# Performance work log

Measured on AMD Instinct MI355X. Metric: run time of the kernel, lower is better.

The kernel has to match this reference:

```python
import jax, jax.numpy as jnp
import numpy as np

ORDER = 256
THETA = 23.0
HIDDEN = 512
INPUT_DIM = 256
BATCH = 8192
TIMESTEPS = 23
LEAKY_SLOPE = 0.2  # tf.nn.leaky_relu default alpha


def _expm_np(M):
    # scaling-and-squaring + Taylor series, float64 numpy (replaces scipy expm)
    n = M.shape[0]
    nrm = np.linalg.norm(M, 1)
    s = max(0, int(np.ceil(np.log2(max(nrm, 1e-30)))) + 1)
    Ms = M / (2.0 ** s)
    E = np.eye(n)
    term = np.eye(n)
    for k in range(1, 30):
        term = term @ Ms / k
        E = E + term
    for _ in range(s):
        E = E @ E
    return E


def get_state_space_matrices(order, theta):
    Q = np.arange(order, dtype=np.float64)
    R = (2 * Q + 1)[:, None] / theta
    j, i = np.meshgrid(Q, Q)
    A = np.where(i < j, -1, (-1.0) ** (i - j + 1)) * R
    B = (-1.0) ** Q[:, None] * R
    # zero-order-hold discretization with dt=1: expm of augmented matrix
    aug = np.zeros((order + 1, order + 1))
    aug[:order, :order] = A
    aug[:order, order:] = B
    M = _expm_np(aug)
    return M[:order, :order], M[:order, order:]


def setup_inputs() -> dict:
    key = jax.random.key(0)
    ks = jax.random.split(key, 5)
    A_np, B_np = get_state_space_matrices(ORDER, THETA)

    def glorot(k, shape):
        lim = np.sqrt(6.0 / (shape[0] + shape[1]))
        return jax.random.uniform(k, shape, jnp.float32, -lim, lim)

    return {
        "inputs": jax.random.normal(ks[0], (BATCH, TIMESTEPS, INPUT_DIM), jnp.float32),
        "A": jnp.asarray(A_np, jnp.float32),          # [order, order]
        "B": jnp.asarray(B_np, jnp.float32),          # [order, 1]
        "W_h": glorot(ks[1], (HIDDEN, HIDDEN)),
        "W_m": glorot(ks[2], (HIDDEN, ORDER)),
        "W_x": glorot(ks[3], (INPUT_DIM, HIDDEN)),
        "e_x": glorot(ks[4], (INPUT_DIM, 1)),
    }


def reference(inputs, A, B, W_h, W_m, W_x, e_x):
    batch = inputs.shape[0]
    Bv = B[:, 0]  # [order]

    def step(carry, x_t):  # x_t: [batch, input_dim]
        h, m = carry  # h: [batch, hidden], m: [batch, order]
        u = x_t @ e_x  # [batch, 1]
        m_new = m @ A.T + u * Bv[None, :]          # [batch, order]
        pre = x_t @ W_x + h @ W_h.T + m_new @ W_m.T  # [batch, hidden]
        h_new = jnp.where(pre >= 0, pre, LEAKY_SLOPE * pre)
        return (h_new, m_new), h_new

    h0 = jnp.zeros((batch, W_h.shape[0]), inputs.dtype)
    m0 = jnp.zeros((batch, A.shape[0]), inputs.dtype)
    xs = jnp.transpose(inputs, (1, 0, 2))  # [T, batch, input_dim]
    _, hs = jax.lax.scan(step, (h0, m0), xs)
    return jnp.transpose(hs, (1, 0, 2))  # [batch, T, hidden]
```

## Files before the change

### kernel.cpp

```cpp
#include <hip/hip_runtime.h>

#define T_STEPS 23
#define ORD 256
#define HID 512
#define IN_DIM 256
#define NBATCH 8192
#define SLOPE 0.2f
#define LDH (T_STEPS * HID)
#define ROWS 32

__device__ __forceinline__ float lrelu(float x) { return x >= 0.f ? x : SLOPE * x; }

__device__ __forceinline__ ushort f2bf(float x) {
    unsigned u = __float_as_uint(x);
    u += 0x7fffu + ((u >> 16) & 1u);
    return (ushort)(u >> 16);
}
__device__ __forceinline__ float bf2f(ushort h) { return __uint_as_float((unsigned)h << 16); }

typedef __attribute__((ext_vector_type(8))) short bf16x8;
typedef __attribute__((ext_vector_type(4))) float f32x4;

__device__ __forceinline__ f32x4 nt_load4(const float* p) {
    return __builtin_nontemporal_load((const f32x4*)p);
}
__device__ __forceinline__ void nt_store4(float* p, f32x4 v) {
    __builtin_nontemporal_store(v, (f32x4*)p);
}

__global__ void vchain_kernel(const float* __restrict__ A,
                              const float* __restrict__ Bv,
                              float* __restrict__ V) {
    __shared__ float v[ORD];
    int i = threadIdx.x;
    v[i] = Bv[i];
    __syncthreads();
    for (int k = 0; k < T_STEPS; ++k) {
        V[k * ORD + i] = v[i];
        float a = 0.f;
        const float4* ar = (const float4*)(A + i * ORD);
        const float4* vr = (const float4*)v;
        #pragma unroll 8
        for (int t = 0; t < ORD / 4; ++t) {
            float4 a4 = ar[t];
            float4 v4 = vr[t];
            a += a4.x * v4.x + a4.y * v4.y + a4.z * v4.z + a4.w * v4.w;
        }
        __syncthreads();
        v[i] = a;
        __syncthreads();
    }
}

__global__ void wtab_kernel(const float* __restrict__ Wm,
                            const float* __restrict__ V,
                            float* __restrict__ wtab) {
    __shared__ float vs[ORD];
    int k = blockIdx.x;
    int j = blockIdx.y * 64 + threadIdx.x;
    ((float4*)vs)[threadIdx.x] = ((const float4*)(V + k * ORD))[threadIdx.x];
    __syncthreads();
    float a = 0.f;
    const float4* wr = (const float4*)(Wm + j * ORD);
    const float4* vr = (const float4*)vs;
    #pragma unroll 8
    for (int i = 0; i < ORD / 4; ++i) {
        float4 w4 = wr[i];
        float4 v4 = vr[i];
        a += w4.x * v4.x + w4.y * v4.y + w4.z * v4.z + w4.w * v4.w;
    }
    wtab[k * HID + j] = a;
}

__global__ void u_kernel(const float* __restrict__ X,
                         const float* __restrict__ ex,
                         float* __restrict__ u) {
    int row = blockIdx.x * 4 + (threadIdx.x >> 6);
    int lane = threadIdx.x & 63;
    const float4* xp = (const float4*)(X + (size_t)row * IN_DIM);
    const float4* ep = (const float4*)ex;
    float4 x4 = xp[lane];
    float4 e4 = ep[lane];
    float acc = x4.x * e4.x + x4.y * e4.y + x4.z * e4.z + x4.w * e4.w;
    #pragma unroll
    for (int off = 32; off; off >>= 1) acc += __shfl_down(acc, off);
    if (lane == 0) u[row] = acc;
}

__global__ __launch_bounds__(256) void gemm_xwx(const float* __restrict__ X,
                                                const float* __restrict__ Wx,
                                                float* __restrict__ out) {
    __shared__ float As[16][68];
    __shared__ float Bs[16][68];
    int tid = threadIdx.x;
    int row0 = blockIdx.x * 64;
    int col0 = blockIdx.y * 64;
    int tx = tid & 15, ty = tid >> 4;
    int am = tid >> 2, ak4 = tid & 3;
    float acc[4][4] = {};
    for (int k0 = 0; k0 < 256; k0 += 16) {
        float4 av = *(const float4*)(X + (size_t)(row0 + am) * IN_DIM + k0 + ak4 * 4);
        float4 bv = *(const float4*)(Wx + (size_t)(k0 + ty) * HID + col0 + tx * 4);
        __syncthreads();
        As[ak4 * 4 + 0][am] = av.x;
        As[ak4 * 4 + 1][am] = av.y;
        As[ak4 * 4 + 2][am] = av.z;
        As[ak4 * 4 + 3][am] = av.w;
        *(float4*)&Bs[ty][tx * 4] = bv;
        __syncthreads();
        #pragma unroll
        for (int kk = 0; kk < 16; ++kk) {
            float4 a4 = *(const float4*)&As[kk][ty * 4];
            float4 b4 = *(const float4*)&Bs[kk][tx * 4];
            float a[4] = {a4.x, a4.y, a4.z, a4.w};
            float b[4] = {b4.x, b4.y, b4.z, b4.w};
            #pragma unroll
            for (int i = 0; i < 4; ++i)
                #pragma unroll
                for (int j = 0; j < 4; ++j)
                    acc[i][j] += a[i] * b[j];
        }
    }
    #pragma unroll
    for (int i = 0; i < 4; ++i) {
        float4 v = make_float4(acc[i][0], acc[i][1], acc[i][2], acc[i][3]);
        *(float4*)(out + (size_t)(row0 + ty * 4 + i) * HID + col0 + tx * 4) = v;
    }
}

__global__ __launch_bounds__(512) void memconv_kernel(const float* __restrict__ u,
                                                      const float* __restrict__ wtab,
                                                      float* __restrict__ out) {
    int b = blockIdx.x, j = threadIdx.x;
    __shared__ float us[T_STEPS];
    if (j < T_STEPS) us[j] = u[b * T_STEPS + j];
    float w[T_STEPS];
    #pragma unroll
    for (int k = 0; k < T_STEPS; ++k) w[k] = wtab[k * HID + j];
    __syncthreads();
    float* ob = out + (size_t)b * LDH + j;
    #pragma unroll
    for (int t = 0; t < T_STEPS; ++t) {
        float acc = 0.f;
        #pragma unroll
        for (int s = 0; s <= t; ++s) acc += us[s] * w[t - s];
        ob[t * HID] += acc;
    }
}

__global__ void whpack_kernel(const float* __restrict__ Wh,
                              ushort* __restrict__ whi,
                              ushort* __restrict__ wlo) {
    int f = blockIdx.x;
    int s = blockIdx.y;
    int l = threadIdx.x;
    int n = f * 16 + (l & 15);
    int k0 = s * 32 + 4 * (l >> 4);
    float4 a = *(const float4*)(Wh + (size_t)n * HID + k0);
    float4 b = *(const float4*)(Wh + (size_t)n * HID + k0 + 16);
    float v[8] = {a.x, a.y, a.z, a.w, b.x, b.y, b.z, b.w};
    unsigned hp[4], lp[4];
    #pragma unroll
    for (int e2 = 0; e2 < 4; ++e2) {
        ushort h0 = f2bf(v[2 * e2]),     h1 = f2bf(v[2 * e2 + 1]);
        ushort l0 = f2bf(v[2 * e2]     - bf2f(h0));
        ushort l1 = f2bf(v[2 * e2 + 1] - bf2f(h1));
        hp[e2] = (unsigned)h0 | ((unsigned)h1 << 16);
        lp[e2] = (unsigned)l0 | ((unsigned)l1 << 16);
    }
    size_t off = ((size_t)(f * 16 + s) * 64 + l) * 8;
    *(uint4*)(whi + off) = make_uint4(hp[0], hp[1], hp[2], hp[3]);
    *(uint4*)(wlo + off) = make_uint4(lp[0], lp[1], lp[2], lp[3]);
}


__device__ __forceinline__ bf16x8 ld_frag(const ushort* base, int o1, int o2) {
    ushort4 p = *(const ushort4*)(base + o1);
    ushort4 q = *(const ushort4*)(base + o2);
    bf16x8 r;
    r[0] = (short)p.x; r[1] = (short)p.y; r[2] = (short)p.z; r[3] = (short)p.w;
    r[4] = (short)q.x; r[5] = (short)q.y; r[6] = (short)q.z; r[7] = (short)q.w;
    return r;
}

__device__ __forceinline__ void store_hilo(ushort* hhi, ushort* hlo, int off, f32x4 v) {
    ushort h0 = f2bf(v[0]), h1 = f2bf(v[1]), h2 = f2bf(v[2]), h3 = f2bf(v[3]);
    *(ushort4*)(hhi + off) = make_ushort4(h0, h1, h2, h3);
    ushort l0 = f2bf(v[0] - bf2f(h0));
    ushort l1 = f2bf(v[1] - bf2f(h1));
    ushort l2 = f2bf(v[2] - bf2f(h2));
    ushort l3 = f2bf(v[3] - bf2f(h3));
    *(ushort4*)(hlo + off) = make_ushort4(l0, l1, l2, l3);
}

__global__ __launch_bounds__(1024) void rec_fused(const ushort* __restrict__ whi,
                                                  const ushort* __restrict__ wlo,
                                                  float* __restrict__ out) {
    __shared__ ushort hbuf[2][2][ROWS * 512];
    const int tid = threadIdx.x;
    const int w  = tid >> 6;
    const int l  = tid & 63;
    const int lm = l & 15;
    const int g  = l >> 4;
    const int row0 = blockIdx.x * ROWS;
    const int xsw = lm << 2;

    float* obase[2];
    obase[0] = out + (size_t)(row0 + lm) * LDH + w * 32 + 4 * g;
    obase[1] = out + (size_t)(row0 + 16 + lm) * LDH + w * 32 + 4 * g;

    #pragma unroll
    for (int bi = 0; bi < 2; ++bi) {
        #pragma unroll
        for (int jf = 0; jf < 2; ++jf) {
            f32x4 vv = nt_load4(obase[bi] + jf * 16);
            vv[0] = lrelu(vv[0]); vv[1] = lrelu(vv[1]);
            vv[2] = lrelu(vv[2]); vv[3] = lrelu(vv[3]);
            nt_store4(obase[bi] + jf * 16, vv);
            int m  = bi * 16 + lm;
            int nb = w * 32 + jf * 16 + 4 * g;
            store_hilo(&hbuf[0][0][0], &hbuf[0][1][0], m * 512 + (nb ^ xsw), vv);
        }
    }

    const ushort* wh_l = whi + (size_t)w * 16384 + (size_t)l * 8;
    const ushort* wl_l = wlo + (size_t)w * 16384 + (size_t)l * 8;

    int buf = 0;
    #pragma unroll 1
    for (int t = 1; t < T_STEPS; ++t) {
        f32x4 pregs[2][2];
        #pragma unroll
        for (int jf = 0; jf < 2; ++jf)
            #pragma unroll
            for (int bi = 0; bi < 2; ++bi)
                pregs[jf][bi] = nt_load4(obase[bi] + t * HID + jf * 16);

        __syncthreads();

        const ushort* hh = &hbuf[buf][0][0];
        const ushort* hl = &hbuf[buf][1][0];
        f32x4 acc[2][2] = {};

        #pragma unroll
        for (int s = 0; s < 16; ++s) {
            bf16x8 ah[2], al[2], bh[2], bl[2];
            #pragma unroll
            for (int jf = 0; jf < 2; ++jf) {
                ah[jf] = *(const bf16x8*)(wh_l + jf * 8192 + s * 512);
                al[jf] = *(const bf16x8*)(wl_l + jf * 8192 + s * 512);
            }
            #pragma unroll
            for (int bi = 0; bi < 2; ++bi) {
                int m  = bi * 16 + lm;
                int o1 = m * 512 + ((s * 32 + 4 * g)      ^ xsw);
                int o2 = m * 512 + ((s * 32 + 16 + 4 * g) ^ xsw);
                bh[bi] = ld_frag(hh, o1, o2);
                bl[bi] = ld_frag(hl, o1, o2);
            }
            #pragma unroll
            for (int jf = 0; jf < 2; ++jf)
                #pragma unroll
                for (int bi = 0; bi < 2; ++bi) {
                    acc[jf][bi] = __builtin_amdgcn_mfma_f32_16x16x32_bf16(ah[jf], bh[bi], acc[jf][bi], 0, 0, 0);
                    acc[jf][bi] = __builtin_amdgcn_mfma_f32_16x16x32_bf16(ah[jf], bl[bi], acc[jf][bi], 0, 0, 0);
                    acc[jf][bi] = __builtin_amdgcn_mfma_f32_16x16x32_bf16(al[jf], bh[bi], acc[jf][bi], 0, 0, 0);
                }
        }

        buf ^= 1;
        #pragma unroll
        for (int jf = 0; jf < 2; ++jf)
            #pragma unroll
            for (int bi = 0; bi < 2; ++bi) {
                f32x4 r;
                r[0] = lrelu(acc[jf][bi][0] + pregs[jf][bi][0]);
                r[1] = lrelu(acc[jf][bi][1] + pregs[jf][bi][1]);
                r[2] = lrelu(acc[jf][bi][2] + pregs[jf][bi][2]);
                r[3] = lrelu(acc[jf][bi][3] + pregs[jf][bi][3]);
                nt_store4(obase[bi] + t * HID + jf * 16, r);
                int m  = bi * 16 + lm;
                int nb = w * 32 + jf * 16 + 4 * g;
                store_hilo(&hbuf[buf][0][0], &hbuf[buf][1][0], m * 512 + (nb ^ xsw), r);
            }
    }
}

extern "C" void kernel_launch(void* const* d_in, const int* in_sizes, int n_in,
                              void* d_out, int out_size, void* d_ws, size_t ws_size,
                              hipStream_t stream) {
    const float* X  = (const float*)d_in[0];
    const float* A  = (const float*)d_in[1];
    const float* Bv = (const float*)d_in[2];
    const float* Wh = (const float*)d_in[3];
    const float* Wm = (const float*)d_in[4];
    const float* Wx = (const float*)d_in[5];
    const float* ex = (const float*)d_in[6];
    float* out = (float*)d_out;

    float* u    = (float*)d_ws;
    float* V    = u + NBATCH * T_STEPS;
    float* wtab = V + T_STEPS * ORD;
    ushort* whp_hi = (ushort*)(wtab + T_STEPS * HID);
    ushort* whp_lo = whp_hi + HID * HID;

    const int nrows = NBATCH * T_STEPS;

    vchain_kernel<<<1, 256, 0, stream>>>(A, Bv, V);
    wtab_kernel<<<dim3(T_STEPS, HID / 64), 64, 0, stream>>>(Wm, V, wtab);
    whpack_kernel<<<dim3(HID / 16, HID / 32), 64, 0, stream>>>(Wh, whp_hi, whp_lo);

    u_kernel<<<nrows / 4, 256, 0, stream>>>(X, ex, u);

    gemm_xwx<<<dim3(nrows / 64, HID / 64), 256, 0, stream>>>(X, Wx, out);

    memconv_kernel<<<NBATCH, HID, 0, stream>>>(u, wtab, out);

    rec_fused<<<NBATCH / ROWS, 1024, 0, stream>>>(whp_hi, whp_lo, out);
}
```

Before: 2.591 ms.

## Replace FP32 input GEMM and memory convolution with fused split-bf16 MFMA kernel

Replaces the scalar FP32 X@W_x GEMM and the separate memory-convolution kernel with one MFMA kernel. It packs W_x and the convolution table into hi/lo bf16 fragments and expresses the causal convolution over u as an extra K=32 MFMA slice per row tile. This removes the read-modify-write pass over the output and moves the dominant GEMM onto matrix cores using a three-product hi/lo split to keep near-FP32 accuracy. The recurrent kernel also changes to 512 threads with wider per-wave column tiles and register double-buffering of W_h fragments, which raises register pressure.

```diff
diff --git a/kernel.cpp b/kernel.cpp
--- a/kernel.cpp
+++ b/kernel.cpp
@@ -8,6 +8,7 @@
 #define SLOPE 0.2f
 #define LDH (T_STEPS * HID)
 #define ROWS 32
+#define PRB 64
 
 __device__ __forceinline__ float lrelu(float x) { return x >= 0.f ? x : SLOPE * x; }
 
@@ -21,9 +22,30 @@
 typedef __attribute__((ext_vector_type(8))) short bf16x8;
 typedef __attribute__((ext_vector_type(4))) float f32x4;
 
-__device__ __forceinline__ f32x4 nt_load4(const float* p) {
-    return __builtin_nontemporal_load((const f32x4*)p);
-}
+
+__device__ __forceinline__ bf16x8 ld_frag(const ushort* base, int o1, int o2) {
+    ushort4 p = *(const ushort4*)(base + o1);
+    ushort4 q = *(const ushort4*)(base + o2);
+    bf16x8 r;
+    r[0] = (short)p.x; r[1] = (short)p.y; r[2] = (short)p.z; r[3] = (short)p.w;
+    r[4] = (short)q.x; r[5] = (short)q.y; r[6] = (short)q.z; r[7] = (short)q.w;
+    return r;
+}
+
+__device__ __forceinline__ void store_hilo(ushort* hhi, ushort* hlo, int off, f32x4 v) {
+    ushort h0 = f2bf(v[0]), h1 = f2bf(v[1]), h2 = f2bf(v[2]), h3 = f2bf(v[3]);
+    *(ushort4*)(hhi + off) = make_ushort4(h0, h1, h2, h3);
+    ushort l0 = f2bf(v[0] - bf2f(h0));
+    ushort l1 = f2bf(v[1] - bf2f(h1));
+    ushort l2 = f2bf(v[2] - bf2f(h2));
+    ushort l3 = f2bf(v[3] - bf2f(h3));
+    *(ushort4*)(hlo + off) = make_ushort4(l0, l1, l2, l3);
+}
+
+__device__ __forceinline__ void split_hilo(float x, ushort& hi, ushort& lo) {
+    hi = f2bf(x); lo = f2bf(x - bf2f(hi));
+}
+
 __device__ __forceinline__ void nt_store4(float* p, f32x4 v) {
     __builtin_nontemporal_store(v, (f32x4*)p);
 }
@@ -87,73 +109,10 @@
     if (lane == 0) u[row] = acc;
 }
 
-__global__ __launch_bounds__(256) void gemm_xwx(const float* __restrict__ X,
-                                                const float* __restrict__ Wx,
-                                                float* __restrict__ out) {
-    __shared__ float As[16][68];
-    __shared__ float Bs[16][68];
-    int tid = threadIdx.x;
-    int row0 = blockIdx.x * 64;
-    int col0 = blockIdx.y * 64;
-    int tx = tid & 15, ty = tid >> 4;
-    int am = tid >> 2, ak4 = tid & 3;
-    float acc[4][4] = {};
-    for (int k0 = 0; k0 < 256; k0 += 16) {
-        float4 av = *(const float4*)(X + (size_t)(row0 + am) * IN_DIM + k0 + ak4 * 4);
-        float4 bv = *(const float4*)(Wx + (size_t)(k0 + ty) * HID + col0 + tx * 4);
-        __syncthreads();
-        As[ak4 * 4 + 0][am] = av.x;
-        As[ak4 * 4 + 1][am] = av.y;
-        As[ak4 * 4 + 2][am] = av.z;
-        As[ak4 * 4 + 3][am] = av.w;
-        *(float4*)&Bs[ty][tx * 4] = bv;
-        __syncthreads();
-        #pragma unroll
-        for (int kk = 0; kk < 16; ++kk) {
-            float4 a4 = *(const float4*)&As[kk][ty * 4];
-            float4 b4 = *(const float4*)&Bs[kk][tx * 4];
-            float a[4] = {a4.x, a4.y, a4.z, a4.w};
-            float b[4] = {b4.x, b4.y, b4.z, b4.w};
-            #pragma unroll
-            for (int i = 0; i < 4; ++i)
-                #pragma unroll
-                for (int j = 0; j < 4; ++j)
-                    acc[i][j] += a[i] * b[j];
-        }
-    }
-    #pragma unroll
-    for (int i = 0; i < 4; ++i) {
-        float4 v = make_float4(acc[i][0], acc[i][1], acc[i][2], acc[i][3]);
-        *(float4*)(out + (size_t)(row0 + ty * 4 + i) * HID + col0 + tx * 4) = v;
-    }
-}
-
-__global__ __launch_bounds__(512) void memconv_kernel(const float* __restrict__ u,
-                                                      const float* __restrict__ wtab,
-                                                      float* __restrict__ out) {
-    int b = blockIdx.x, j = threadIdx.x;
-    __shared__ float us[T_STEPS];
-    if (j < T_STEPS) us[j] = u[b * T_STEPS + j];
-    float w[T_STEPS];
-    #pragma unroll
-    for (int k = 0; k < T_STEPS; ++k) w[k] = wtab[k * HID + j];
-    __syncthreads();
-    float* ob = out + (size_t)b * LDH + j;
-    #pragma unroll
-    for (int t = 0; t < T_STEPS; ++t) {
-        float acc = 0.f;
-        #pragma unroll
-        for (int s = 0; s <= t; ++s) acc += us[s] * w[t - s];
-        ob[t * HID] += acc;
-    }
-}
-
 __global__ void whpack_kernel(const float* __restrict__ Wh,
                               ushort* __restrict__ whi,
                               ushort* __restrict__ wlo) {
-    int f = blockIdx.x;
-    int s = blockIdx.y;
-    int l = threadIdx.x;
+    int f = blockIdx.x, s = blockIdx.y, l = threadIdx.x;
     int n = f * 16 + (l & 15);
     int k0 = s * 32 + 4 * (l >> 4);
     float4 a = *(const float4*)(Wh + (size_t)n * HID + k0);
@@ -162,9 +121,9 @@
     unsigned hp[4], lp[4];
     #pragma unroll
     for (int e2 = 0; e2 < 4; ++e2) {
-        ushort h0 = f2bf(v[2 * e2]),     h1 = f2bf(v[2 * e2 + 1]);
-        ushort l0 = f2bf(v[2 * e2]     - bf2f(h0));
-        ushort l1 = f2bf(v[2 * e2 + 1] - bf2f(h1));
+        ushort h0, l0, h1, l1;
+        split_hilo(v[2 * e2], h0, l0);
+        split_hilo(v[2 * e2 + 1], h1, l1);
         hp[e2] = (unsigned)h0 | ((unsigned)h1 << 16);
         lp[e2] = (unsigned)l0 | ((unsigned)l1 << 16);
     }
@@ -173,104 +132,229 @@
     *(uint4*)(wlo + off) = make_uint4(lp[0], lp[1], lp[2], lp[3]);
 }
 
-
-__device__ __forceinline__ bf16x8 ld_frag(const ushort* base, int o1, int o2) {
-    ushort4 p = *(const ushort4*)(base + o1);
-    ushort4 q = *(const ushort4*)(base + o2);
-    bf16x8 r;
-    r[0] = (short)p.x; r[1] = (short)p.y; r[2] = (short)p.z; r[3] = (short)p.w;
-    r[4] = (short)q.x; r[5] = (short)q.y; r[6] = (short)q.z; r[7] = (short)q.w;
-    return r;
-}
-
-__device__ __forceinline__ void store_hilo(ushort* hhi, ushort* hlo, int off, f32x4 v) {
-    ushort h0 = f2bf(v[0]), h1 = f2bf(v[1]), h2 = f2bf(v[2]), h3 = f2bf(v[3]);
-    *(ushort4*)(hhi + off) = make_ushort4(h0, h1, h2, h3);
-    ushort l0 = f2bf(v[0] - bf2f(h0));
-    ushort l1 = f2bf(v[1] - bf2f(h1));
-    ushort l2 = f2bf(v[2] - bf2f(h2));
-    ushort l3 = f2bf(v[3] - bf2f(h3));
-    *(ushort4*)(hlo + off) = make_ushort4(l0, l1, l2, l3);
-}
-
-__global__ __launch_bounds__(1024) void rec_fused(const ushort* __restrict__ whi,
-                                                  const ushort* __restrict__ wlo,
-                                                  float* __restrict__ out) {
+__global__ void wxpack_kernel(const float* __restrict__ Wx,
+                              ushort* __restrict__ whi,
+                              ushort* __restrict__ wlo) {
+    int f = blockIdx.x, s = blockIdx.y, l = threadIdx.x;
+    int n = f * 16 + (l & 15);
+    ushort hp[8], lp[8];
+    #pragma unroll
+    for (int e = 0; e < 8; ++e) {
+        int k = s * 32 + 4 * (l >> 4) + (e & 3) + 16 * (e >> 2);
+        split_hilo(Wx[(size_t)k * HID + n], hp[e], lp[e]);
+    }
+    size_t off = ((size_t)(f * 8 + s) * 64 + l) * 8;
+    *(uint4*)(whi + off) = *(uint4*)hp;
+    *(uint4*)(wlo + off) = *(uint4*)lp;
+}
+
+__global__ void wtabpack_kernel(const float* __restrict__ wtab,
+                                ushort* __restrict__ whi,
+                                ushort* __restrict__ wlo) {
+    int f = blockIdx.x, l = threadIdx.x;
+    int n = f * 16 + (l & 15);
+    ushort hp[8], lp[8];
+    #pragma unroll
+    for (int e = 0; e < 8; ++e) {
+        int k = 4 * (l >> 4) + (e & 3) + 16 * (e >> 2);
+        float v = (k < T_STEPS) ? wtab[(size_t)k * HID + n] : 0.f;
+        split_hilo(v, hp[e], lp[e]);
+    }
+    size_t off = ((size_t)f * 64 + l) * 8;
+    *(uint4*)(whi + off) = *(uint4*)hp;
+    *(uint4*)(wlo + off) = *(uint4*)lp;
+}
+
+__global__ __launch_bounds__(512, 2) void gemm_pre(const float* __restrict__ X,
+                                                   const float* __restrict__ u,
+                                                   const ushort* __restrict__ wxhi,
+                                                   const ushort* __restrict__ wxlo,
+                                                   const ushort* __restrict__ wthi,
+                                                   const ushort* __restrict__ wtlo,
+                                                   float* __restrict__ out) {
+    __shared__ ushort xs[2][PRB * 256];
+    __shared__ float us_sh[PRB + 22];
+    const int tid = threadIdx.x;
+    const int w = tid >> 6, l = tid & 63, lm = l & 15, g = l >> 4;
+    const int row0 = blockIdx.x * PRB;
+    const int xsw = lm << 2;
+
+    if (tid < PRB + 22) {
+        int idx = row0 - 22 + tid;
+        us_sh[tid] = (idx >= 0) ? u[idx] : 0.f;
+    }
+    {
+        int r = tid >> 3;
+        int c8 = tid & 7;
+        const float4* xrow = (const float4*)(X + (size_t)(row0 + r) * IN_DIM);
+        int xswr = (r & 15) << 2;
+        #pragma unroll
+        for (int i = 0; i < 8; ++i) {
+            float4 v4 = xrow[c8 + i * 8];
+            f32x4 vv; vv[0] = v4.x; vv[1] = v4.y; vv[2] = v4.z; vv[3] = v4.w;
+            int k0 = (c8 + i * 8) * 4;
+            store_hilo(&xs[0][0], &xs[1][0], r * 256 + (k0 ^ xswr), vv);
+        }
+    }
+    __syncthreads();
+
+    f32x4 acc[4][4] = {};
+    const ushort* wxh_l = wxhi + (size_t)w * 16384 + (size_t)l * 8;
+    const ushort* wxl_l = wxlo + (size_t)w * 16384 + (size_t)l * 8;
+
+    #pragma unroll
+    for (int s = 0; s < 8; ++s) {
+        bf16x8 bh[4], bl[4];
+        #pragma unroll
+        for (int bi = 0; bi < 4; ++bi) {
+            int m = bi * 16 + lm;
+            int o1 = m * 256 + ((s * 32 + 4 * g) ^ xsw);
+            int o2 = m * 256 + ((s * 32 + 16 + 4 * g) ^ xsw);
+            bh[bi] = ld_frag(&xs[0][0], o1, o2);
+            bl[bi] = ld_frag(&xs[1][0], o1, o2);
+        }
+        #pragma unroll
+        for (int jf = 0; jf < 4; ++jf) {
+            bf16x8 ah = *(const bf16x8*)(wxh_l + jf * 4096 + s * 512);
+            bf16x8 al = *(const bf16x8*)(wxl_l + jf * 4096 + s * 512);
+            #pragma unroll
+            for (int bi = 0; bi < 4; ++bi) {
+                acc[jf][bi] = __builtin_amdgcn_mfma_f32_16x16x32_bf16(ah, bh[bi], acc[jf][bi], 0, 0, 0);
+                acc[jf][bi] = __builtin_amdgcn_mfma_f32_16x16x32_bf16(ah, bl[bi], acc[jf][bi], 0, 0, 0);
+                acc[jf][bi] = __builtin_amdgcn_mfma_f32_16x16x32_bf16(al, bh[bi], acc[jf][bi], 0, 0, 0);
+            }
+        }
+    }
+
+    {
+        bf16x8 bh[4], bl[4];
+        #pragma unroll
+        for (int bi = 0; bi < 4; ++bi) {
+            int rloc = bi * 16 + lm;
+            int t = (row0 + rloc) % T_STEPS;
+            #pragma unroll
+            for (int e = 0; e < 8; ++e) {
+                int k = 4 * g + (e & 3) + 16 * (e >> 2);
+                float v = (k <= t) ? us_sh[rloc + 22 - k] : 0.f;
+                ushort hi, lo;
+                split_hilo(v, hi, lo);
+                bh[bi][e] = (short)hi;
+                bl[bi][e] = (short)lo;
+            }
+        }
+        #pragma unroll
+        for (int jf = 0; jf < 4; ++jf) {
+            bf16x8 ah = *(const bf16x8*)(wthi + (size_t)(w * 4 + jf) * 512 + l * 8);
+            bf16x8 al = *(const bf16x8*)(wtlo + (size_t)(w * 4 + jf) * 512 + l * 8);
+            #pragma unroll
+            for (int bi = 0; bi < 4; ++bi) {
+                acc[jf][bi] = __builtin_amdgcn_mfma_f32_16x16x32_bf16(ah, bh[bi], acc[jf][bi], 0, 0, 0);
+                acc[jf][bi] = __builtin_amdgcn_mfma_f32_16x16x32_bf16(ah, bl[bi], acc[jf][bi], 0, 0, 0);
+                acc[jf][bi] = __builtin_amdgcn_mfma_f32_16x16x32_bf16(al, bh[bi], acc[jf][bi], 0, 0, 0);
+            }
+        }
+    }
+
+    #pragma unroll
+    for (int bi = 0; bi < 4; ++bi) {
+        float* op = out + (size_t)(row0 + bi * 16 + lm) * HID + w * 64 + 4 * g;
+        #pragma unroll
+        for (int jf = 0; jf < 4; ++jf) {
+            float4 v = make_float4(acc[jf][bi][0], acc[jf][bi][1], acc[jf][bi][2], acc[jf][bi][3]);
+            *(float4*)(op + jf * 16) = v;
+        }
+    }
+}
+
+__global__ __launch_bounds__(512, 2) void rec_fused(const ushort* __restrict__ whi,
+                                                    const ushort* __restrict__ wlo,
+                                                    float* __restrict__ out) {
     __shared__ ushort hbuf[2][2][ROWS * 512];
     const int tid = threadIdx.x;
-    const int w  = tid >> 6;
-    const int l  = tid & 63;
-    const int lm = l & 15;
-    const int g  = l >> 4;
+    const int w = tid >> 6, l = tid & 63, lm = l & 15, g = l >> 4;
     const int row0 = blockIdx.x * ROWS;
     const int xsw = lm << 2;
 
     float* obase[2];
-    obase[0] = out + (size_t)(row0 + lm) * LDH + w * 32 + 4 * g;
-    obase[1] = out + (size_t)(row0 + 16 + lm) * LDH + w * 32 + 4 * g;
+    obase[0] = out + (size_t)(row0 + lm) * LDH + w * 64 + 4 * g;
+    obase[1] = out + (size_t)(row0 + 16 + lm) * LDH + w * 64 + 4 * g;
 
     #pragma unroll
     for (int bi = 0; bi < 2; ++bi) {
         #pragma unroll
-        for (int jf = 0; jf < 2; ++jf) {
-            f32x4 vv = nt_load4(obase[bi] + jf * 16);
+        for (int jf = 0; jf < 4; ++jf) {
+            f32x4 vv = *(f32x4*)(obase[bi] + jf * 16);
             vv[0] = lrelu(vv[0]); vv[1] = lrelu(vv[1]);
             vv[2] = lrelu(vv[2]); vv[3] = lrelu(vv[3]);
             nt_store4(obase[bi] + jf * 16, vv);
-            int m  = bi * 16 + lm;
-            int nb = w * 32 + jf * 16 + 4 * g;
+            int m = bi * 16 + lm;
+            int nb = w * 64 + jf * 16 + 4 * g;
             store_hilo(&hbuf[0][0][0], &hbuf[0][1][0], m * 512 + (nb ^ xsw), vv);
         }
     }
 
-    const ushort* wh_l = whi + (size_t)w * 16384 + (size_t)l * 8;
-    const ushort* wl_l = wlo + (size_t)w * 16384 + (size_t)l * 8;
+    const ushort* wh_l = whi + (size_t)w * 32768 + (size_t)l * 8;
+    const ushort* wl_l = wlo + (size_t)w * 32768 + (size_t)l * 8;
 
     int buf = 0;
     #pragma unroll 1
     for (int t = 1; t < T_STEPS; ++t) {
-        f32x4 pregs[2][2];
-        #pragma unroll
-        for (int jf = 0; jf < 2; ++jf)
+        f32x4 pregs[4][2];
+        #pragma unroll
+        for (int jf = 0; jf < 4; ++jf)
             #pragma unroll
             for (int bi = 0; bi < 2; ++bi)
-                pregs[jf][bi] = nt_load4(obase[bi] + t * HID + jf * 16);
+                pregs[jf][bi] = *(f32x4*)(obase[bi] + t * HID + jf * 16);
+
+        bf16x8 ahc[4], alc[4];
+        #pragma unroll
+        for (int jf = 0; jf < 4; ++jf) {
+            ahc[jf] = *(const bf16x8*)(wh_l + jf * 8192);
+            alc[jf] = *(const bf16x8*)(wl_l + jf * 8192);
+        }
 
         __syncthreads();
 
         const ushort* hh = &hbuf[buf][0][0];
         const ushort* hl = &hbuf[buf][1][0];
-        f32x4 acc[2][2] = {};
+        f32x4 acc[4][2] = {};
 
         #pragma unroll
         for (int s = 0; s < 16; ++s) {
-            bf16x8 ah[2], al[2], bh[2], bl[2];
-            #pragma unroll
-            for (int jf = 0; jf < 2; ++jf) {
-                ah[jf] = *(const bf16x8*)(wh_l + jf * 8192 + s * 512);
-                al[jf] = *(const bf16x8*)(wl_l + jf * 8192 + s * 512);
-            }
+            bf16x8 ahn[4], aln[4];
+            if (s < 15) {
+                #pragma unroll
+                for (int jf = 0; jf < 4; ++jf) {
+                    ahn[jf] = *(const bf16x8*)(wh_l + jf * 8192 + (s + 1) * 512);
+                    aln[jf] = *(const bf16x8*)(wl_l + jf * 8192 + (s + 1) * 512);
+                }
+            }
+            bf16x8 bh[2], bl[2];
             #pragma unroll
             for (int bi = 0; bi < 2; ++bi) {
-                int m  = bi * 16 + lm;
-                int o1 = m * 512 + ((s * 32 + 4 * g)      ^ xsw);
+                int m = bi * 16 + lm;
+                int o1 = m * 512 + ((s * 32 + 4 * g) ^ xsw);
                 int o2 = m * 512 + ((s * 32 + 16 + 4 * g) ^ xsw);
                 bh[bi] = ld_frag(hh, o1, o2);
                 bl[bi] = ld_frag(hl, o1, o2);
             }
             #pragma unroll
-            for (int jf = 0; jf < 2; ++jf)
+            for (int jf = 0; jf < 4; ++jf)
                 #pragma unroll
                 for (int bi = 0; bi < 2; ++bi) {
-                    acc[jf][bi] = __builtin_amdgcn_mfma_f32_16x16x32_bf16(ah[jf], bh[bi], acc[jf][bi], 0, 0, 0);
-                    acc[jf][bi] = __builtin_amdgcn_mfma_f32_16x16x32_bf16(ah[jf], bl[bi], acc[jf][bi], 0, 0, 0);
-                    acc[jf][bi] = __builtin_amdgcn_mfma_f32_16x16x32_bf16(al[jf], bh[bi], acc[jf][bi], 0, 0, 0);
+                    acc[jf][bi] = __builtin_amdgcn_mfma_f32_16x16x32_bf16(ahc[jf], bh[bi], acc[jf][bi], 0, 0, 0);
+                    acc[jf][bi] = __builtin_amdgcn_mfma_f32_16x16x32_bf16(ahc[jf], bl[bi], acc[jf][bi], 0, 0, 0);
+                    acc[jf][bi] = __builtin_amdgcn_mfma_f32_16x16x32_bf16(alc[jf], bh[bi], acc[jf][bi], 0, 0, 0);
                 }
+            if (s < 15) {
+                #pragma unroll
+                for (int jf = 0; jf < 4; ++jf) { ahc[jf] = ahn[jf]; alc[jf] = aln[jf]; }
+            }
         }
 
         buf ^= 1;
         #pragma unroll
-        for (int jf = 0; jf < 2; ++jf)
+        for (int jf = 0; jf < 4; ++jf)
             #pragma unroll
             for (int bi = 0; bi < 2; ++bi) {
                 f32x4 r;
@@ -279,8 +363,8 @@
                 r[2] = lrelu(acc[jf][bi][2] + pregs[jf][bi][2]);
                 r[3] = lrelu(acc[jf][bi][3] + pregs[jf][bi][3]);
                 nt_store4(obase[bi] + t * HID + jf * 16, r);
-                int m  = bi * 16 + lm;
-                int nb = w * 32 + jf * 16 + 4 * g;
+                int m = bi * 16 + lm;
+                int nb = w * 64 + jf * 16 + 4 * g;
                 store_hilo(&hbuf[buf][0][0], &hbuf[buf][1][0], m * 512 + (nb ^ xsw), r);
             }
     }
@@ -298,23 +382,28 @@
     const float* ex = (const float*)d_in[6];
     float* out = (float*)d_out;
 
+    const int nrows = NBATCH * T_STEPS;
+
     float* u    = (float*)d_ws;
-    float* V    = u + NBATCH * T_STEPS;
+    float* V    = u + nrows;
     float* wtab = V + T_STEPS * ORD;
     ushort* whp_hi = (ushort*)(wtab + T_STEPS * HID);
     ushort* whp_lo = whp_hi + HID * HID;
-
-    const int nrows = NBATCH * T_STEPS;
+    ushort* wxp_hi = whp_lo + HID * HID;
+    ushort* wxp_lo = wxp_hi + IN_DIM * HID;
+    ushort* wtp_hi = wxp_lo + IN_DIM * HID;
+    ushort* wtp_lo = wtp_hi + 32 * 512;
 
     vchain_kernel<<<1, 256, 0, stream>>>(A, Bv, V);
     wtab_kernel<<<dim3(T_STEPS, HID / 64), 64, 0, stream>>>(Wm, V, wtab);
+    wtabpack_kernel<<<32, 64, 0, stream>>>(wtab, wtp_hi, wtp_lo);
     whpack_kernel<<<dim3(HID / 16, HID / 32), 64, 0, stream>>>(Wh, whp_hi, whp_lo);
+    wxpack_kernel<<<dim3(HID / 16, IN_DIM / 32), 64, 0, stream>>>(Wx, wxp_hi, wxp_lo);
 
     u_kernel<<<nrows / 4, 256, 0, stream>>>(X, ex, u);
 
-    gemm_xwx<<<dim3(nrows / 64, HID / 64), 256, 0, stream>>>(X, Wx, out);
-
-    memconv_kernel<<<NBATCH, HID, 0, stream>>>(u, wtab, out);
-
-    rec_fused<<<NBATCH / ROWS, 1024, 0, stream>>>(whp_hi, whp_lo, out);
-}
+    gemm_pre<<<nrows / PRB, 512, 0, stream>>>(X, u, wxp_hi, wxp_lo,
+                                              wtp_hi, wtp_lo, out);
+
+    rec_fused<<<NBATCH / ROWS, 512, 0, stream>>>(whp_hi, whp_lo, out);
+}
```

New measurement: 2.092 ms. 19.3% less time.
